# Performance work log

Hardware: AMD Instinct MI355X
Metric: run time of the kernel (lower is better)

The kernel has to match this reference:

```python
import jax, jax.numpy as jnp
import numpy as np

# e3nn normalize2mom gain for tanh (1/sqrt(E[tanh(z)^2]), z~N(0,1))
TANH_GAIN = 1.5927116870880127
B, M_IN, M_HID, M_OUT = 8192, 64, 128, 64

_W_SPECS = {
    'b1_l1_w0': (64, 64), 'b1_l1_w1': (64, 64), 'b1_l2_w0': (64, 64), 'b1_l2_w1': (64, 64),
    'b1_tp_ss': (64, 64, 128), 'b1_tp_vv': (64, 64, 128), 'b1_tp_sv': (64, 64, 128), 'b1_tp_vs': (64, 64, 128),
    'b1_g_ws': (128, 128), 'b1_g_wg': (128, 128), 'b1_g_wv': (128, 128),
    'b1_o_w0': (128, 128), 'b1_o_w1': (128, 128),
    'b2_l1_w0': (128, 128), 'b2_l1_w1': (128, 128), 'b2_l2_w0': (128, 128), 'b2_l2_w1': (128, 128),
    'b2_tp_ss': (128, 128, 128), 'b2_tp_vv': (128, 128, 128), 'b2_tp_sv': (128, 128, 128), 'b2_tp_vs': (128, 128, 128),
    'b2_g_ws': (128, 128), 'b2_g_wg': (128, 128), 'b2_g_wv': (128, 128),
    'b2_o_w0': (128, 128), 'b2_o_w1': (128, 128),
    'f_w0': (128, 64), 'f_w1': (128, 64),
}


def setup_inputs() -> dict:
    key = jax.random.key(0)
    ks = jax.random.split(key, len(_W_SPECS) + 1)
    d = {'x': jax.random.normal(ks[0], (B, M_IN + 3 * M_IN), jnp.float32)}
    for i, (name, shp) in enumerate(_W_SPECS.items()):
        d[name] = jax.random.normal(ks[i + 1], shp, jnp.float32)  # e3nn weights ~ N(0,1)
    return d


def _lin(s, v, w0, w1):
    # o3.Linear on 'Mx0e+Mx1o': per-irrep block matmul, path_normalization='element' -> 1/sqrt(fan_in)
    c = 1.0 / np.sqrt(w0.shape[0])
    return (s @ w0) * c, jnp.einsum('bui,uw->bwi', v, w1) * c


def _tp(s1, v1, s2, v2, wss, wvv, wsv, wvs):
    # FullyConnectedTensorProduct, irrep_normalization='component', path_normalization='element'.
    # Two uvw paths feed each output irrep -> path_weight = sqrt(dim_out / (2*M*M)).
    # CG values: w3j(0,0,0)=1; w3j(0,1,1)=delta/sqrt(3); w3j(1,0,1)=delta/sqrt(3); w3j(1,1,0)=delta/sqrt(3).
    M = s1.shape[-1]
    c = 1.0 / (M * np.sqrt(2.0))
    s = c * jnp.einsum('bu,bv,uvw->bw', s1, s2, wss) \
        + (c / np.sqrt(3.0)) * jnp.einsum('bui,bvi,uvw->bw', v1, v2, wvv)
    v = c * (jnp.einsum('bu,bvi,uvw->bwi', s1, v2, wsv)
             + jnp.einsum('bui,bv,uvw->bwi', v1, s2, wvs))
    return s, v


def _gate(s, v, ws, wg, wv):
    # LearnableGate: o3.Linear to (scalars | gate scalars | vectors), then e3nn Gate
    # (tanh w/ normalize2mom gain on scalars and gates; elementwise gate*vector has unit path weight).
    c = 1.0 / np.sqrt(ws.shape[0])
    sl = (s @ ws) * c
    g = (s @ wg) * c
    vl = jnp.einsum('bui,uw->bwi', v, wv) * c
    return TANH_GAIN * jnp.tanh(sl), (TANH_GAIN * jnp.tanh(g))[..., None] * vl


def _block(s, v, p):
    l1w0, l1w1, l2w0, l2w1, wss, wvv, wsv, wvs, gws, gwg, gwv, ow0, ow1 = p
    s1, v1 = _lin(s, v, l1w0, l1w1)
    s2, v2 = _lin(s, v, l2w0, l2w1)
    s, v = _tp(s1, v1, s2, v2, wss, wvv, wsv, wvs)
    s, v = _gate(s, v, gws, gwg, gwv)
    return _lin(s, v, ow0, ow1)


def _forward(x, *w):
    s = x[:, :M_IN]
    v = x[:, M_IN:].reshape(x.shape[0], M_IN, 3)
    s, v = _block(s, v, w[0:13])
    s, v = _block(s, v, w[13:26])
    s, v = _lin(s, v, w[26], w[27])
    return jnp.concatenate([s, v.reshape(v.shape[0], -1)], axis=-1)


def reference(x, b1_l1_w0, b1_l1_w1, b1_l2_w0, b1_l2_w1, b1_tp_ss, b1_tp_vv, b1_tp_sv, b1_tp_vs, b1_g_ws, b1_g_wg, b1_g_wv, b1_o_w0, b1_o_w1, b2_l1_w0, b2_l1_w1, b2_l2_w0, b2_l2_w1, b2_tp_ss, b2_tp_vv, b2_tp_sv, b2_tp_vs, b2_g_ws, b2_g_wg, b2_g_wv, b2_o_w0, b2_o_w1, f_w0, f_w1):
    return _forward(x, b1_l1_w0, b1_l1_w1, b1_l2_w0, b1_l2_w1, b1_tp_ss, b1_tp_vv, b1_tp_sv, b1_tp_vs, b1_g_ws, b1_g_wg, b1_g_wv, b1_o_w0, b1_o_w1, b2_l1_w0, b2_l1_w1, b2_l2_w0, b2_l2_w1, b2_tp_ss, b2_tp_vv, b2_tp_sv, b2_tp_vs, b2_g_ws, b2_g_wg, b2_g_wv, b2_o_w0, b2_o_w1, f_w0, f_w1)
```

## Files before the change

kernel.cpp:

```cpp
#include <hip/hip_runtime.h>
#include <math.h>

typedef _Float16 f16;
typedef __attribute__((ext_vector_type(8))) _Float16 half8;
typedef __attribute__((ext_vector_type(4))) _Float16 half4;
typedef __attribute__((ext_vector_type(4))) float floatx4;

#define NB 8192

struct ConvJob { const float* src; f16* dst; int K; int N; int ucount; float scale; int swz; };
struct ConvJobs { ConvJob j[28]; };

__global__ void convert_w(ConvJobs JJ) {
    ConvJob jb = JJ.j[blockIdx.z];
    int u = blockIdx.x;
    if (u >= jb.ucount) return;
    __shared__ f16 tile[128 * 136];
    const int K = jb.K, N = jb.N;
    const int npad = N + 8;
    const int nsh = (N == 128) ? 7 : 6;
    const int ksh = (K == 128) ? 7 : 6;
    const float* src = jb.src + (size_t)u * K * N;
    for (int idx = threadIdx.x; idx < K * N; idx += 256) {
        int k = idx >> nsh, n = idx & (N - 1);
        tile[k * npad + n] = (f16)(src[idx] * jb.scale);
    }
    __syncthreads();
    f16* dst = jb.dst + (size_t)u * N * K;
    for (int idx = threadIdx.x; idx < N * K; idx += 256) {
        int n = idx >> ksh, rem = idx & (K - 1);
        int g2 = rem >> 3, jj = rem & 7;
        int g = jb.swz ? (g2 ^ (n & jb.swz)) : g2;
        int k = g * 8 + jj;
        dst[idx] = tile[k * npad + n];
    }
}

__global__ void x_to_planes(const float* __restrict__ x, f16* s_p, f16* v0, f16* v1, f16* v2) {
    int t = blockIdx.x * 256 + threadIdx.x;
    if (t >= NB * 64) return;
    int b = t >> 6, u = t & 63;
    const float* xr = x + (size_t)b * 256;
    s_p[t] = (f16)xr[u];
    v0[t] = (f16)xr[64 + 3 * u + 0];
    v1[t] = (f16)xr[64 + 3 * u + 1];
    v2[t] = (f16)xr[64 + 3 * u + 2];
}

struct TpJob { const f16* p; const f16* q; const f16* w; float* out; int pstride; int qstride; };
struct TpJobs { TpJob j[10]; };

template <int M>
__launch_bounds__(256, (M == 128) ? 3 : 4)
__global__ void tp_unit(TpJobs JJ) {
    TpJob jb = JJ.j[blockIdx.z];
    constexpr int KC = M / 32;
    constexpr int GM = M / 8 - 1;
    constexpr int SLABH = 64 * M;
    constexpr int PIECES = SLABH / 8;
    constexpr int IPW = PIECES / 256;
    constexpr int SLABFULL = 128 * M;
    __shared__ f16 w_lds[2][SLABH];
    const int tid = threadIdx.x, lane = tid & 63, wave = tid >> 6;
    const int wm = wave & 1, wn = wave >> 1;
    const int l15 = lane & 15, quad = lane >> 4;
    const int rowBase = blockIdx.x * 128;
    const int colBase = blockIdx.y * 64;

    half8 qf[4][KC];
    int prow[4];
    #pragma unroll
    for (int t = 0; t < 4; t++) {
        int row = rowBase + wm * 64 + t * 16 + l15;
        prow[t] = row;
        const f16* qr = jb.q + (size_t)row * jb.qstride;
        #pragma unroll
        for (int c = 0; c < KC; c++) qf[t][c] = *(const half8*)(qr + c * 32 + quad * 8);
    }
    floatx4 acc[4][2];
    #pragma unroll
    for (int a = 0; a < 4; a++)
        #pragma unroll
        for (int b = 0; b < 2; b++) acc[a][b] = (floatx4){0.f, 0.f, 0.f, 0.f};

    int rd_off[2][KC];
    #pragma unroll
    for (int nt = 0; nt < 2; nt++) {
        int nl = wn * 32 + nt * 16 + l15;
        #pragma unroll
        for (int c = 0; c < KC; c++) {
            int g = c * 4 + quad;
            rd_off[nt][c] = nl * M + ((g ^ (nl & GM)) << 3);
        }
    }

    const int wpBase = wave * (PIECES / 4);
    const f16* wsrc0 = jb.w + (size_t)colBase * M + (size_t)(wpBase + lane) * 8;
    auto stage = [&](int u, int buf) {
        const f16* src = wsrc0 + (size_t)u * SLABFULL;
        f16* dst = &w_lds[buf][0] + (size_t)wpBase * 8;
        #pragma unroll
        for (int i = 0; i < IPW; i++) {
            __builtin_amdgcn_global_load_lds(
                (const __attribute__((address_space(1))) void*)(src + i * 64 * 8),
                (__attribute__((address_space(3))) void*)(dst + i * 64 * 8),
                16, 0, 0);
        }
    };

    stage(0, 0);
    __syncthreads();

    for (int uc = 0; uc < M / 8; uc++) {
        half8 pcur[4];
        #pragma unroll
        for (int t = 0; t < 4; t++)
            pcur[t] = *(const half8*)(jb.p + (size_t)prow[t] * jb.pstride + uc * 8);
        #pragma unroll
        for (int j = 0; j < 8; j++) {
            const int u = uc * 8 + j;
            const int cur = j & 1;
            if (j != 7 || uc != M / 8 - 1) stage(u + 1, cur ^ 1);
            #pragma unroll
            for (int c = 0; c < KC; c++) {
                half8 af[4];
                #pragma unroll
                for (int t = 0; t < 4; t++) {
                    f16 pv = pcur[t][j];
                    half8 p8 = {pv, pv, pv, pv, pv, pv, pv, pv};
                    af[t] = qf[t][c] * p8;
                }
                #pragma unroll
                for (int nt = 0; nt < 2; nt++) {
                    half8 bf = *(const half8*)&w_lds[cur][rd_off[nt][c]];
                    #pragma unroll
                    for (int t = 0; t < 4; t++)
                        acc[t][nt] = __builtin_amdgcn_mfma_f32_16x16x32_f16(af[t], bf, acc[t][nt], 0, 0, 0);
                }
            }
            __syncthreads();
        }
    }
    #pragma unroll
    for (int t = 0; t < 4; t++)
        #pragma unroll
        for (int nt = 0; nt < 2; nt++) {
            int col = colBase + wn * 32 + nt * 16 + l15;
            float* orow = jb.out + (size_t)(rowBase + wm * 64 + t * 16 + quad * 4) * 128 + col;
            #pragma unroll
            for (int r = 0; r < 4; r++) orow[(size_t)r * 128] = acc[t][nt][r];
        }
}

struct SmallJob { const f16* A; const f16* W; char* out; int astride; int ostride;
                  int ocol; int cstride; int mode; int Njob; int ny;
                  const f16* Amul; int mstride;
                  const float* red0; const float* red1; const float* red2; const float* red3;
                  int nred; };
struct SmallJobs { SmallJob j[4]; };

template <int K>
__launch_bounds__(256, 2)
__global__ void small_gemm(SmallJobs JJ) {
    SmallJob jb = JJ.j[blockIdx.z];
    if ((int)blockIdx.y >= jb.ny) return;
    constexpr int KC = K / 32;
    constexpr int NP = K + 8;
    constexpr int PR = K / 8;
    constexpr int PPT = 128 * K / 8 / 256;
    __shared__ f16 w_lds[128 * NP];
    const int tid = threadIdx.x, lane = tid & 63, wave = tid >> 6;
    const int wm = wave & 1, wn = wave >> 1;
    const int l15 = lane & 15, quad = lane >> 4;
    const int rowBase = blockIdx.x * 64;
    const int nBase = blockIdx.y * 128;

    #pragma unroll
    for (int t = 0; t < PPT; t++) {
        int idx = t * 256 + tid;
        int r = idx / PR, pc = idx % PR;
        int4 v = {0, 0, 0, 0};
        if (nBase + r < jb.Njob)
            v = *(const int4*)(jb.W + (size_t)(nBase + r) * K + pc * 8);
        *(int4*)&w_lds[r * NP + pc * 8] = v;
    }
    half8 qf[2][KC];
    for (int t = 0; t < 2; t++) {
        int row = rowBase + wm * 32 + t * 16 + l15;
        if (jb.nred) {
            #pragma unroll
            for (int c = 0; c < KC; c++) {
                size_t boff = (size_t)row * 128 + c * 32 + quad * 8;
                floatx4 s0 = *(const floatx4*)(jb.red0 + boff);
                floatx4 s1 = *(const floatx4*)(jb.red0 + boff + 4);
                if (jb.nred > 1) { s0 += *(const floatx4*)(jb.red1 + boff); s1 += *(const floatx4*)(jb.red1 + boff + 4); }
                if (jb.nred > 2) { s0 += *(const floatx4*)(jb.red2 + boff); s1 += *(const floatx4*)(jb.red2 + boff + 4); }
                if (jb.nred > 3) { s0 += *(const floatx4*)(jb.red3 + boff); s1 += *(const floatx4*)(jb.red3 + boff + 4); }
                qf[t][c] = (half8){(f16)s0.x, (f16)s0.y, (f16)s0.z, (f16)s0.w,
                                   (f16)s1.x, (f16)s1.y, (f16)s1.z, (f16)s1.w};
            }
        } else {
            const f16* ar = jb.A + (size_t)row * jb.astride;
            #pragma unroll
            for (int c = 0; c < KC; c++) qf[t][c] = *(const half8*)(ar + c * 32 + quad * 8);
        }
        if (jb.Amul) {
            const f16* mr = jb.Amul + (size_t)row * jb.mstride;
            #pragma unroll
            for (int c = 0; c < KC; c++) qf[t][c] = qf[t][c] * *(const half8*)(mr + c * 32 + quad * 8);
        }
    }
    floatx4 acc[2][4];
    #pragma unroll
    for (int a = 0; a < 2; a++)
        #pragma unroll
        for (int b = 0; b < 4; b++) acc[a][b] = (floatx4){0.f, 0.f, 0.f, 0.f};
    __syncthreads();
    #pragma unroll
    for (int c = 0; c < KC; c++)
        #pragma unroll
        for (int nt = 0; nt < 4; nt++) {
            half8 bf = *(const half8*)&w_lds[(wn * 64 + nt * 16 + l15) * NP + c * 32 + quad * 8];
            #pragma unroll
            for (int t = 0; t < 2; t++)
                acc[t][nt] = __builtin_amdgcn_mfma_f32_16x16x32_f16(qf[t][c], bf, acc[t][nt], 0, 0, 0);
        }
    const float GAIN = 1.5927116870880127f;
    #pragma unroll
    for (int t = 0; t < 2; t++)
        #pragma unroll
        for (int nt = 0; nt < 4; nt++) {
            int col = nBase + wn * 64 + nt * 16 + l15;
            if (col >= jb.Njob) continue;
            int rowB = rowBase + wm * 32 + t * 16 + quad * 4;
            #pragma unroll
            for (int r = 0; r < 4; r++) {
                float v = acc[t][nt][r];
                size_t ro = (size_t)(rowB + r) * jb.ostride;
                if (jb.mode == 0)      ((f16*)jb.out)[ro + jb.ocol + col] = (f16)v;
                else if (jb.mode == 1) ((f16*)jb.out)[ro + jb.ocol + col] = (f16)(GAIN * tanhf(v));
                else                   ((float*)jb.out)[ro + jb.ocol + (size_t)col * jb.cstride] = v;
            }
        }
}

extern "C" void kernel_launch(void* const* d_in, const int* in_sizes, int n_in,
                              void* d_out, int out_size, void* d_ws, size_t ws_size,
                              hipStream_t stream) {
    const float* x = (const float*)d_in[0];
    const float* W_IN[28];
    for (int i = 0; i < 28; i++) W_IN[i] = (const float*)d_in[1 + i];

    char* base = (char*)d_ws;
    size_t off = 0;
    auto alloc = [&](size_t bytes) -> char* {
        char* p = base + off;
        off += (bytes + 255) & ~(size_t)255;
        return p;
    };
    const size_t S128 = (size_t)NB * 128;

    f16* Wl12_b1_s = (f16*)alloc(8192 * 2);
    f16* Wl12_b1_v = (f16*)alloc(8192 * 2);
    f16* Wl12_b2_s = (f16*)alloc(32768 * 2);
    f16* Wl12_b2_v = (f16*)alloc(32768 * 2);
    f16* Wtp_b1[4]; for (int i = 0; i < 4; i++) Wtp_b1[i] = (f16*)alloc((size_t)64 * 128 * 64 * 2);
    f16* Wtp_b2[4]; for (int i = 0; i < 4; i++) Wtp_b2[i] = (f16*)alloc((size_t)128 * 128 * 128 * 2);
    f16* Wg_b1_sg = (f16*)alloc(32768 * 2);
    f16* Wg_b1_v  = (f16*)alloc(16384 * 2);
    f16* Wg_b2_sg = (f16*)alloc(32768 * 2);
    f16* Wg_b2_v  = (f16*)alloc(16384 * 2);
    f16* Wo_b1_s = (f16*)alloc(16384 * 2);
    f16* Wo_b1_v = (f16*)alloc(16384 * 2);
    f16* Wo_b2_s = (f16*)alloc(16384 * 2);
    f16* Wo_b2_v = (f16*)alloc(16384 * 2);
    f16* Wf_s = (f16*)alloc(8192 * 2);
    f16* Wf_v = (f16*)alloc(8192 * 2);
    f16* s_p = (f16*)alloc((size_t)NB * 64 * 2);
    f16* v_p[3]; for (int i = 0; i < 3; i++) v_p[i] = (f16*)alloc((size_t)NB * 64 * 2);
    f16* Breg = (f16*)alloc((size_t)4 * NB * 256 * 2);
    float* Part = (float*)alloc((size_t)10 * S128 * 4);
    f16* Ereg = (f16*)alloc((size_t)5 * S128 * 2);
    f16* Freg = (f16*)alloc((size_t)4 * S128 * 2);
    (void)ws_size; (void)in_sizes; (void)n_in; (void)out_size;

    const float c_l1 = 0.125f;
    const float c128 = 0.088388347648318447f;
    const float c1 = 1.0f / (64.0f * 1.4142135623730951f);
    const float c2 = 1.0f / (128.0f * 1.4142135623730951f);
    const float i3 = 0.57735026918962584f;

    ConvJobs CJ;
    int jn = 0;
    auto CV = [&](const float* s, f16* d, int K, int N, int uc, float sc, int swz) {
        CJ.j[jn++] = ConvJob{s, d, K, N, uc, sc, swz};
    };
    CV(W_IN[0], Wl12_b1_s, 64, 64, 1, c_l1, 0);  CV(W_IN[2], Wl12_b1_s + 4096, 64, 64, 1, c_l1, 0);
    CV(W_IN[1], Wl12_b1_v, 64, 64, 1, c_l1, 0);  CV(W_IN[3], Wl12_b1_v + 4096, 64, 64, 1, c_l1, 0);
    CV(W_IN[13], Wl12_b2_s, 128, 128, 1, c128, 0); CV(W_IN[15], Wl12_b2_s + 16384, 128, 128, 1, c128, 0);
    CV(W_IN[14], Wl12_b2_v, 128, 128, 1, c128, 0); CV(W_IN[16], Wl12_b2_v + 16384, 128, 128, 1, c128, 0);
    CV(W_IN[4], Wtp_b1[0], 64, 128, 64, c1, 7);  CV(W_IN[5], Wtp_b1[1], 64, 128, 64, c1 * i3, 7);
    CV(W_IN[6], Wtp_b1[2], 64, 128, 64, c1, 7);  CV(W_IN[7], Wtp_b1[3], 64, 128, 64, c1, 7);
    CV(W_IN[17], Wtp_b2[0], 128, 128, 128, c2, 15); CV(W_IN[18], Wtp_b2[1], 128, 128, 128, c2 * i3, 15);
    CV(W_IN[19], Wtp_b2[2], 128, 128, 128, c2, 15); CV(W_IN[20], Wtp_b2[3], 128, 128, 128, c2, 15);
    CV(W_IN[8], Wg_b1_sg, 128, 128, 1, c128, 0);  CV(W_IN[9], Wg_b1_sg + 16384, 128, 128, 1, c128, 0);
    CV(W_IN[10], Wg_b1_v, 128, 128, 1, c128, 0);
    CV(W_IN[21], Wg_b2_sg, 128, 128, 1, c128, 0); CV(W_IN[22], Wg_b2_sg + 16384, 128, 128, 1, c128, 0);
    CV(W_IN[23], Wg_b2_v, 128, 128, 1, c128, 0);
    CV(W_IN[11], Wo_b1_s, 128, 128, 1, c128, 0);  CV(W_IN[12], Wo_b1_v, 128, 128, 1, c128, 0);
    CV(W_IN[24], Wo_b2_s, 128, 128, 1, c128, 0);  CV(W_IN[25], Wo_b2_v, 128, 128, 1, c128, 0);
    CV(W_IN[26], Wf_s, 128, 64, 1, c128, 0);      CV(W_IN[27], Wf_v, 128, 64, 1, c128, 0);
    convert_w<<<dim3(128, 1, 28), 256, 0, stream>>>(CJ);

    x_to_planes<<<NB * 64 / 256, 256, 0, stream>>>(x, s_p, v_p[0], v_p[1], v_p[2]);

    auto SJ = [](const f16* A, const f16* W, void* out, int as, int os, int oc, int cs,
                 int mode, int Nj, int ny, const f16* Amul, int ms) {
        return SmallJob{A, W, (char*)out, as, os, oc, cs, mode, Nj, ny, Amul, ms,
                        nullptr, nullptr, nullptr, nullptr, 0};
    };

    f16* s12 = Breg;
    f16* v12[3]; for (int i = 0; i < 3; i++) v12[i] = Breg + (size_t)(1 + i) * NB * 128;
    f16* sg_gg = Ereg;
    f16* vl[3]; for (int i = 0; i < 3; i++) vl[i] = Ereg + 2 * S128 + i * S128;
    f16* s_o = Freg; f16* v_o[3]; for (int i = 0; i < 3; i++) v_o[i] = Freg + (1 + i) * S128;

    {
        SmallJobs J;
        J.j[0] = SJ(s_p, Wl12_b1_s, s12, 64, 128, 0, 1, 0, 128, 1, nullptr, 0);
        for (int i = 0; i < 3; i++) J.j[1 + i] = SJ(v_p[i], Wl12_b1_v, v12[i], 64, 128, 0, 1, 0, 128, 1, nullptr, 0);
        small_gemm<64><<<dim3(128, 1, 4), 256, 0, stream>>>(J);
    }
    {
        TpJobs J;
        J.j[0] = TpJob{s12, s12 + 64, Wtp_b1[0], Part + 0 * S128, 128, 128};
        for (int i = 0; i < 3; i++) J.j[1 + i] = TpJob{v12[i], v12[i] + 64, Wtp_b1[1], Part + (1 + i) * S128, 128, 128};
        for (int i = 0; i < 3; i++) J.j[4 + i] = TpJob{s12, v12[i] + 64, Wtp_b1[2], Part + (4 + i) * S128, 128, 128};
        for (int i = 0; i < 3; i++) J.j[7 + i] = TpJob{v12[i], s12 + 64, Wtp_b1[3], Part + (7 + i) * S128, 128, 128};
        tp_unit<64><<<dim3(64, 2, 10), 256, 0, stream>>>(J);
    }
    {
        SmallJobs J;
        J.j[0] = SmallJob{nullptr, Wg_b1_sg, (char*)sg_gg, 128, 256, 0, 1, 1, 256, 2, nullptr, 0,
                          Part + 0 * S128, Part + 1 * S128, Part + 2 * S128, Part + 3 * S128, 4};
        for (int i = 0; i < 3; i++)
            J.j[1 + i] = SmallJob{nullptr, Wg_b1_v, (char*)vl[i], 128, 128, 0, 1, 0, 128, 1, nullptr, 0,
                                  Part + (4 + i) * S128, Part + (7 + i) * S128, nullptr, nullptr, 2};
        small_gemm<128><<<dim3(128, 2, 4), 256, 0, stream>>>(J);
    }
    {
        SmallJobs J;
        J.j[0] = SJ(sg_gg, Wo_b1_s, s_o, 256, 128, 0, 1, 0, 128, 1, nullptr, 0);
        for (int i = 0; i < 3; i++) J.j[1 + i] = SJ(vl[i], Wo_b1_v, v_o[i], 128, 128, 0, 1, 0, 128, 1, sg_gg + 128, 256);
        small_gemm<128><<<dim3(128, 1, 4), 256, 0, stream>>>(J);
    }
    f16* s12b = Breg;
    f16* v12b[3]; for (int i = 0; i < 3; i++) v12b[i] = Breg + (size_t)(1 + i) * NB * 256;
    {
        SmallJobs J;
        J.j[0] = SJ(s_o, Wl12_b2_s, s12b, 128, 256, 0, 1, 0, 256, 2, nullptr, 0);
        for (int i = 0; i < 3; i++) J.j[1 + i] = SJ(v_o[i], Wl12_b2_v, v12b[i], 128, 256, 0, 1, 0, 256, 2, nullptr, 0);
        small_gemm<128><<<dim3(128, 2, 4), 256, 0, stream>>>(J);
    }
    {
        TpJobs J;
        J.j[0] = TpJob{s12b, s12b + 128, Wtp_b2[0], Part + 0 * S128, 256, 256};
        for (int i = 0; i < 3; i++) J.j[1 + i] = TpJob{v12b[i], v12b[i] + 128, Wtp_b2[1], Part + (1 + i) * S128, 256, 256};
        for (int i = 0; i < 3; i++) J.j[4 + i] = TpJob{s12b, v12b[i] + 128, Wtp_b2[2], Part + (4 + i) * S128, 256, 256};
        for (int i = 0; i < 3; i++) J.j[7 + i] = TpJob{v12b[i], s12b + 128, Wtp_b2[3], Part + (7 + i) * S128, 256, 256};
        tp_unit<128><<<dim3(64, 2, 10), 256, 0, stream>>>(J);
    }
    {
        SmallJobs J;
        J.j[0] = SmallJob{nullptr, Wg_b2_sg, (char*)sg_gg, 128, 256, 0, 1, 1, 256, 2, nullptr, 0,
                          Part + 0 * S128, Part + 1 * S128, Part + 2 * S128, Part + 3 * S128, 4};
        for (int i = 0; i < 3; i++)
            J.j[1 + i] = SmallJob{nullptr, Wg_b2_v, (char*)vl[i], 128, 128, 0, 1, 0, 128, 1, nullptr, 0,
                                  Part + (4 + i) * S128, Part + (7 + i) * S128, nullptr, nullptr, 2};
        small_gemm<128><<<dim3(128, 2, 4), 256, 0, stream>>>(J);
    }
    {
        SmallJobs J;
        J.j[0] = SJ(sg_gg, Wo_b2_s, s_o, 256, 128, 0, 1, 0, 128, 1, nullptr, 0);
        for (int i = 0; i < 3; i++) J.j[1 + i] = SJ(vl[i], Wo_b2_v, v_o[i], 128, 128, 0, 1, 0, 128, 1, sg_gg + 128, 256);
        small_gemm<128><<<dim3(128, 1, 4), 256, 0, stream>>>(J);
    }
    {
        SmallJobs J;
        J.j[0] = SJ(s_o, Wf_s, d_out, 128, 256, 0, 1, 2, 64, 1, nullptr, 0);
        for (int i = 0; i < 3; i++) J.j[1 + i] = SJ(v_o[i], Wf_v, d_out, 128, 256, 64 + i, 3, 2, 64, 1, nullptr, 0);
        small_gemm<128><<<dim3(128, 1, 4), 256, 0, stream>>>(J);
    }
}
```

Baseline: 637.5 us.

## Switch tensor-product kernel to 32x32x16 MFMA with per-wave row strips

Restructures the tp_unit kernel so each wave owns a 32-row strip across all 64 columns and uses 32x32x16 MFMA instead of 16x16x32 tiles. The per-u scaling of the q fragments by p drops from four rows-tiles to one per wave, which cuts VALU multiply work and register footprint, and the kernel raises occupancy to 5 blocks per CU. It also sets wave priority around the MFMA loop. The trade-off is that every wave now reads the full 64-column weight slab from LDS instead of half of it, which doubles LDS read traffic per wave.

Result: slower. 671.5 us (+5.3%).

```diff
diff --git a/kernel.cpp b/kernel.cpp
--- a/kernel.cpp
+++ b/kernel.cpp
@@ -3,8 +3,8 @@
 
 typedef _Float16 f16;
 typedef __attribute__((ext_vector_type(8))) _Float16 half8;
-typedef __attribute__((ext_vector_type(4))) _Float16 half4;
 typedef __attribute__((ext_vector_type(4))) float floatx4;
+typedef __attribute__((ext_vector_type(16))) float floatx16;
 
 #define NB 8192
 
@@ -51,10 +51,10 @@
 struct TpJobs { TpJob j[10]; };
 
 template <int M>
-__launch_bounds__(256, (M == 128) ? 3 : 4)
+__launch_bounds__(256, 5)
 __global__ void tp_unit(TpJobs JJ) {
     TpJob jb = JJ.j[blockIdx.z];
-    constexpr int KC = M / 32;
+    constexpr int KC = M / 16;
     constexpr int GM = M / 8 - 1;
     constexpr int SLABH = 64 * M;
     constexpr int PIECES = SLABH / 8;
@@ -62,34 +62,30 @@
     constexpr int SLABFULL = 128 * M;
     __shared__ f16 w_lds[2][SLABH];
     const int tid = threadIdx.x, lane = tid & 63, wave = tid >> 6;
-    const int wm = wave & 1, wn = wave >> 1;
-    const int l15 = lane & 15, quad = lane >> 4;
+    const int l31 = lane & 31, khalf = lane >> 5;
     const int rowBase = blockIdx.x * 128;
     const int colBase = blockIdx.y * 64;
 
-    half8 qf[4][KC];
-    int prow[4];
-    #pragma unroll
-    for (int t = 0; t < 4; t++) {
-        int row = rowBase + wm * 64 + t * 16 + l15;
-        prow[t] = row;
-        const f16* qr = jb.q + (size_t)row * jb.qstride;
-        #pragma unroll
-        for (int c = 0; c < KC; c++) qf[t][c] = *(const half8*)(qr + c * 32 + quad * 8);
-    }
-    floatx4 acc[4][2];
-    #pragma unroll
-    for (int a = 0; a < 4; a++)
-        #pragma unroll
-        for (int b = 0; b < 2; b++) acc[a][b] = (floatx4){0.f, 0.f, 0.f, 0.f};
+    const int prow = rowBase + wave * 32 + l31;
+    half8 qf[KC];
+    {
+        const f16* qr = jb.q + (size_t)prow * jb.qstride;
+        #pragma unroll
+        for (int c = 0; c < KC; c++) qf[c] = *(const half8*)(qr + c * 16 + khalf * 8);
+    }
+    floatx16 acc[2];
+    #pragma unroll
+    for (int t = 0; t < 2; t++)
+        #pragma unroll
+        for (int r = 0; r < 16; r++) acc[t][r] = 0.f;
 
     int rd_off[2][KC];
     #pragma unroll
     for (int nt = 0; nt < 2; nt++) {
-        int nl = wn * 32 + nt * 16 + l15;
+        int nl = nt * 32 + l31;
         #pragma unroll
         for (int c = 0; c < KC; c++) {
-            int g = c * 4 + quad;
+            int g = c * 2 + khalf;
             rd_off[nt][c] = nl * M + ((g ^ (nl & GM)) << 3);
         }
     }
@@ -112,44 +108,40 @@
     __syncthreads();
 
     for (int uc = 0; uc < M / 8; uc++) {
-        half8 pcur[4];
-        #pragma unroll
-        for (int t = 0; t < 4; t++)
-            pcur[t] = *(const half8*)(jb.p + (size_t)prow[t] * jb.pstride + uc * 8);
+        half8 pcur = *(const half8*)(jb.p + (size_t)prow * jb.pstride + uc * 8);
         #pragma unroll
         for (int j = 0; j < 8; j++) {
             const int u = uc * 8 + j;
-            const int cur = j & 1;
-            if (j != 7 || uc != M / 8 - 1) stage(u + 1, cur ^ 1);
+            const int cur = u & 1;
+            if (u < M - 1) stage(u + 1, cur ^ 1);
+            const f16* wl = &w_lds[cur][0];
+            __builtin_amdgcn_s_setprio(1);
             #pragma unroll
             for (int c = 0; c < KC; c++) {
-                half8 af[4];
-                #pragma unroll
-                for (int t = 0; t < 4; t++) {
-                    f16 pv = pcur[t][j];
-                    half8 p8 = {pv, pv, pv, pv, pv, pv, pv, pv};
-                    af[t] = qf[t][c] * p8;
-                }
+                f16 pv = pcur[j];
+                half8 p8 = {pv, pv, pv, pv, pv, pv, pv, pv};
+                half8 af = qf[c] * p8;
                 #pragma unroll
                 for (int nt = 0; nt < 2; nt++) {
-                    half8 bf = *(const half8*)&w_lds[cur][rd_off[nt][c]];
-                    #pragma unroll
-                    for (int t = 0; t < 4; t++)
-                        acc[t][nt] = __builtin_amdgcn_mfma_f32_16x16x32_f16(af[t], bf, acc[t][nt], 0, 0, 0);
+                    half8 bf = *(const half8*)(wl + rd_off[nt][c]);
+                    acc[nt] = __builtin_amdgcn_mfma_f32_32x32x16_f16(af, bf, acc[nt], 0, 0, 0);
                 }
             }
+            __builtin_amdgcn_s_setprio(0);
             __syncthreads();
         }
     }
     #pragma unroll
-    for (int t = 0; t < 4; t++)
-        #pragma unroll
-        for (int nt = 0; nt < 2; nt++) {
-            int col = colBase + wn * 32 + nt * 16 + l15;
-            float* orow = jb.out + (size_t)(rowBase + wm * 64 + t * 16 + quad * 4) * 128 + col;
-            #pragma unroll
-            for (int r = 0; r < 4; r++) orow[(size_t)r * 128] = acc[t][nt][r];
-        }
+    for (int nt = 0; nt < 2; nt++) {
+        int col = colBase + nt * 32 + l31;
+        int rbase = rowBase + wave * 32 + 4 * khalf;
+        float* o = jb.out + (size_t)rbase * 128 + col;
+        #pragma unroll
+        for (int r = 0; r < 16; r++) {
+            int row_off = (r & 3) + 8 * (r >> 2);
+            o[(size_t)row_off * 128] = acc[nt][r];
+        }
+    }
 }
 
 struct SmallJob { const f16* A; const f16* W; char* out; int astride; int ostride;
```
